# Optimization experiments

Measured on AMD Instinct MI355X. Metric: run time of the kernel, lower is better.

Reference implementation:

```python
import jax, jax.numpy as jnp
import numpy as np
import math

DIM = 768
NUM_HEADS = 16
PERHEAD = DIM // NUM_HEADS  # 48
B, T = 4, 2048


def setup_inputs() -> dict:
    key = jax.random.key(0)
    k_x, k_wi, k_bi, k_wo, k_bo = jax.random.split(key, 5)
    s_in = 1.0 / math.sqrt(DIM)
    return {
        "x": jax.random.normal(k_x, (B, T, DIM), dtype=jnp.float32),
        # linear_in: y = x @ w_in + b_in, w_in: (DIM, 3*DIM)
        "w_in": jax.random.uniform(k_wi, (DIM, 3 * DIM), jnp.float32, -s_in, s_in),
        "b_in": jax.random.uniform(k_bi, (3 * DIM,), jnp.float32, -s_in, s_in),
        "w_out": jax.random.uniform(k_wo, (DIM, DIM), jnp.float32, -s_in, s_in),
        "b_out": jax.random.uniform(k_bo, (DIM,), jnp.float32, -s_in, s_in),
    }


def reference(x, w_in, b_in, w_out, b_out):
    bs, tok, _ = x.shape
    qkv = x @ w_in + b_in                                   # (B, T, 3*DIM)
    # Faithful to torch: reshape to (B, T, H, 3*ph), move heads, chunk last dim.
    qkv = qkv.reshape(bs, tok, NUM_HEADS, 3 * PERHEAD)
    qkv = jnp.transpose(qkv, (0, 2, 1, 3))                  # (B, H, T, 3*ph)
    q, k, v = jnp.split(qkv, 3, axis=-1)                    # each (B, H, T, ph)
    scale = 1.0 / math.sqrt(PERHEAD)
    scores = jnp.einsum("bhqd,bhkd->bhqk", q, k) * scale    # (B, H, T, T)
    attn = jax.nn.softmax(scores, axis=-1)
    # dropout p=0.0 (eval) -> identity
    out = jnp.einsum("bhqk,bhkd->bhqd", attn, v)            # (B, H, T, ph)
    out = jnp.transpose(out, (0, 2, 1, 3)).reshape(bs, tok, DIM)
    return out @ w_out + b_out
```

## Files before the change

kernel.cpp:

```cpp
#include <hip/hip_runtime.h>
#include <hip/hip_bf16.h>
#include <math.h>

typedef __attribute__((ext_vector_type(8))) short short8;
typedef __attribute__((ext_vector_type(4))) float floatx4;
typedef __hip_bfloat16 bf16;

#define DIM 768
#define NHEADS 16
#define PH 48
#define VROWS 49
#define BATCH 4
#define SEQ 2048
#define MTOK (BATCH*SEQ)
#define NQKV (3*DIM)
#define NQK (2*DIM)
#define LOG2E 1.44269504088896f
#define CFAC (0.14433756729740643f * LOG2E)

#define NB_CAST   6144
#define NB_TWIN   1728
#define NB_TWOUT  576
#define NB_MISC   140

__device__ __forceinline__ void cp16(void* dst, const void* src) {
    *(float4*)dst = *(const float4*)src;
}
__device__ __forceinline__ unsigned short f2us(float v) {
    bf16 b = __float2bfloat16(v);
    return *(unsigned short*)&b;
}
__device__ __forceinline__ float us2f(unsigned short u) {
    bf16 b = *(bf16*)&u;
    return __bfloat162float(b);
}
__device__ __forceinline__ void gload_lds16(const bf16* g, bf16* l) {
    __builtin_amdgcn_global_load_lds(
        (const __attribute__((address_space(1))) unsigned int*)g,
        (__attribute__((address_space(3))) unsigned int*)l, 16, 0, 0);
}
__device__ __forceinline__ bool sniff_f32(const unsigned short* __restrict__ x) {
    float v = us2f(x[threadIdx.x & 63]);
    int bad = !(fabsf(v) < 64.0f);
    return __any(bad) != 0;
}

__global__ __launch_bounds__(256) void prep_all(
    const void* __restrict__ x, const void* __restrict__ w_in,
    const void* __restrict__ w_out, const void* __restrict__ bin,
    const void* __restrict__ bout,
    bf16* __restrict__ xb, bf16* __restrict__ winT, bf16* __restrict__ woutT,
    float* __restrict__ bi, float* __restrict__ bo, bf16* __restrict__ Vt)
{
    __shared__ bf16 tile[32][33];
    const int bid = blockIdx.x, tid = threadIdx.x;
    const bool f32 = sniff_f32((const unsigned short*)x);

    if (bid < NB_CAST) {
        int i = bid * 256 + tid;
        if (f32) {
            float4 v = ((const float4*)x)[i];
            ushort4 o;
            o.x = f2us(v.x); o.y = f2us(v.y); o.z = f2us(v.z); o.w = f2us(v.w);
            ((ushort4*)xb)[i] = o;
        } else {
            ((ushort4*)xb)[i] = ((const ushort4*)x)[i];
        }
    } else if (bid < NB_CAST + NB_TWIN + NB_TWOUT) {
        const void* in; bf16* out; int R, C, tt;
        if (bid < NB_CAST + NB_TWIN) {
            in = w_in; out = winT; R = DIM; C = NQKV; tt = bid - NB_CAST;
        } else {
            in = w_out; out = woutT; R = DIM; C = DIM; tt = bid - NB_CAST - NB_TWIN;
        }
        int ctiles = C / 32;
        int c0 = (tt % ctiles) * 32, r0 = (tt / ctiles) * 32;
        int tx = tid & 31, ty = tid >> 5;
#pragma unroll
        for (int j = 0; j < 4; j++) {
            size_t idx = (size_t)(r0 + ty + 8*j) * C + c0 + tx;
            float v = f32 ? ((const float*)in)[idx]
                          : us2f(((const unsigned short*)in)[idx]);
            tile[ty + 8*j][tx] = __float2bfloat16(v);
        }
        __syncthreads();
#pragma unroll
        for (int j = 0; j < 4; j++)
            out[(size_t)(c0 + ty + 8*j) * R + r0 + tx] = tile[tx][ty + 8*j];
    } else {
        int t = (bid - (NB_CAST + NB_TWIN + NB_TWOUT)) * 256 + tid;
        if (t < NQKV) {
            bi[t] = f32 ? ((const float*)bin)[t] : us2f(((const unsigned short*)bin)[t]);
        } else if (t < NQKV + DIM) {
            int j = t - NQKV;
            bo[j] = f32 ? ((const float*)bout)[j] : us2f(((const unsigned short*)bout)[j]);
        } else {
            int k = t - (NQKV + DIM);
            int bh = k >> 9, pos = (k & 511) * 4;
            bf16* dst = Vt + ((size_t)bh * VROWS + 48) * SEQ + pos;
            ushort4 ones;
            ones.x = ones.y = ones.z = ones.w = f2us(1.0f);
            *(ushort4*)dst = ones;
        }
    }
}

template<int N, int MODE>
__global__ __launch_bounds__(256) void gemm_bias(
    const bf16* __restrict__ A, const bf16* __restrict__ BT,
    const float* __restrict__ bias, void* __restrict__ C0, bf16* __restrict__ Vt,
    const unsigned short* __restrict__ xraw)
{
    constexpr int K = 768;
    __shared__ __align__(16) bf16 smem[2 * 128 * 32];
    bf16* As = smem;
    bf16* Bs = smem + 128 * 32;
    const bool out_f32 = (MODE == 2) && sniff_f32(xraw);
    const int tid = threadIdx.x;
    const int id = blockIdx.x;
    const int m0 = (id & 63) * 128, n0 = (id >> 6) * 128;
    const int w = tid >> 6, lane = tid & 63, lq = lane >> 4, ln = lane & 15;
    const int wr = w & 1, wc = w >> 1;

    const int rl0 = w * 32 + (lane >> 2);
    const int rl1 = rl0 + 16;
    const int ssw = ((lane >> 2) ^ (lane >> 4)) & 3;
    const int cm = (lane & 3) ^ ssw;
    const bf16* gA0 = A + (size_t)(m0 + rl0) * K + cm * 8;
    const bf16* gA1 = A + (size_t)(m0 + rl1) * K + cm * 8;
    const bf16* gB0 = BT + (size_t)(n0 + rl0) * K + cm * 8;
    const bf16* gB1 = BT + (size_t)(n0 + rl1) * K + cm * 8;
    bf16* lA0 = &As[(w * 32 + 0) * 32];
    bf16* lA1 = &As[(w * 32 + 16) * 32];
    bf16* lB0 = &Bs[(w * 32 + 0) * 32];
    bf16* lB1 = &Bs[(w * 32 + 16) * 32];

    const int rsw = (ln ^ (ln >> 2)) & 3;
    const int rchunk = (lq ^ rsw) * 8;

    floatx4 zero4 = {0.f, 0.f, 0.f, 0.f};
    floatx4 acc[4][4];
#pragma unroll
    for (int mi = 0; mi < 4; mi++)
#pragma unroll
        for (int nj = 0; nj < 4; nj++) acc[mi][nj] = zero4;

    for (int k0 = 0; k0 < K; k0 += 32) {
        gload_lds16(gA0, lA0);
        gload_lds16(gA1, lA1);
        gload_lds16(gB0, lB0);
        gload_lds16(gB1, lB1);
        gA0 += 32; gA1 += 32; gB0 += 32; gB1 += 32;
        __syncthreads();

        short8 a[4], b[4];
#pragma unroll
        for (int mi = 0; mi < 4; mi++)
            a[mi] = *(const short8*)&As[(wr * 64 + 16 * mi + ln) * 32 + rchunk];
#pragma unroll
        for (int nj = 0; nj < 4; nj++)
            b[nj] = *(const short8*)&Bs[(wc * 64 + 16 * nj + ln) * 32 + rchunk];
#pragma unroll
        for (int mi = 0; mi < 4; mi++)
#pragma unroll
            for (int nj = 0; nj < 4; nj++)
                acc[mi][nj] = __builtin_amdgcn_mfma_f32_16x16x32_bf16(
                    a[mi], b[nj], acc[mi][nj], 0, 0, 0);
        __syncthreads();
    }
    bf16 (*VLs)[136] = (bf16(*)[136])smem;

#pragma unroll
    for (int nj = 0; nj < 4; nj++) {
        int n = n0 + wc * 64 + 16 * nj + ln;
        float bv = bias[n];
        if (MODE == 2) {
#pragma unroll
            for (int mi = 0; mi < 4; mi++)
#pragma unroll
                for (int i = 0; i < 4; i++) {
                    size_t off = (size_t)(m0 + wr * 64 + 16 * mi + 4 * lq + i) * N + n;
                    float val = acc[mi][nj][i] + bv;
                    if (out_f32) ((float*)C0)[off] = val;
                    else         ((bf16*)C0)[off] = __float2bfloat16(val);
                }
        } else {
            int h = n / 144, r = n - 144 * h;
            if (r < 96) {
                float sc = (r < 48) ? CFAC : 1.0f;
#pragma unroll
                for (int mi = 0; mi < 4; mi++)
#pragma unroll
                    for (int i = 0; i < 4; i++) {
                        size_t off = (size_t)(m0 + wr * 64 + 16 * mi + 4 * lq + i) * NQK
                                     + h * 96 + r;
                        ((bf16*)C0)[off] = __float2bfloat16((acc[mi][nj][i] + bv) * sc);
                    }
            } else {
                int d = r - 96;
#pragma unroll
                for (int mi = 0; mi < 4; mi++)
#pragma unroll
                    for (int i = 0; i < 4; i++)
                        VLs[d][wr * 64 + 32 * (mi >> 1) + 8 * lq + 4 * (mi & 1) + i] =
                            __float2bfloat16(acc[mi][nj][i] + bv);
            }
        }
    }

    if (MODE == 1) {
        __syncthreads();
        const int bidx = m0 >> 11, tok0 = m0 & 2047;
#pragma unroll
        for (int s = 0; s < 3; s++) {
            int idx = tid + 256 * s;
            int d = idx >> 4, ch = idx & 15;
            int h = (n0 + 31 - d) / 144;
            int n = 144 * h + 96 + d;
            if (n >= n0 && n < n0 + 128) {
                bf16* dst = Vt + ((size_t)(bidx * NHEADS + h) * VROWS + d) * SEQ
                            + tok0 + ch * 8;
                *(float4*)dst = *(const float4*)&VLs[d][ch * 8];
            }
        }
    }
}

__global__ __launch_bounds__(256, 2) void attn_fused(
    const bf16* __restrict__ QK, const bf16* __restrict__ Vt, bf16* __restrict__ O)
{
    __shared__ bf16 Ks[2][64][72];
    __shared__ bf16 VsT[2][64][72];

    const int tid = threadIdx.x;
    const int id = blockIdx.x;
    const int g = id & 63, qt = id >> 6;
    const int h = g & 15, b = g >> 4;
    const int w = tid >> 6, lane = tid & 63, lq = lane >> 4, ln = lane & 15;
    const size_t rowbase = (size_t)b * SEQ;
    const int q0 = qt * 256;
    const int hoff = h * 96;
    const bf16* Vth = Vt + (size_t)(b * NHEADS + h) * VROWS * SEQ;

    const bf16 bzero = __float2bfloat16(0.f);
    for (int idx = tid; idx < 2048; idx += 256) {
        int bb = idx >> 10, r = (idx >> 4) & 63, c = idx & 15;
        Ks[bb][r][48 + c] = bzero;
    }

    short8 qa0[4], qa1[4];
    short8 zero8 = {0, 0, 0, 0, 0, 0, 0, 0};
#pragma unroll
    for (int f = 0; f < 4; f++) {
        const bf16* qrow = QK + (rowbase + q0 + 64*f + 16*w + ln) * NQK + hoff;
        qa0[f] = *(const short8*)(qrow + lq * 8);
        qa1[f] = (lq < 2) ? *(const short8*)(qrow + 32 + lq * 8) : zero8;
    }

    const int kr0a = tid / 6, kc0a = tid % 6;
    const int kr1a = (tid + 256) / 6, kc1a = (tid + 256) % 6;
    const char* kg0 = (const char*)(QK + (rowbase + kr0a) * NQK + hoff + 48) + kc0a * 16;
    const char* kg1 = (const char*)(QK + (rowbase + kr1a) * NQK + hoff + 48) + kc1a * 16;
    bf16* kd0 = &Ks[0][kr0a][kc0a * 8];
    bf16* kd1 = &Ks[0][kr1a & 63][kc1a * 8];
    const bool kact = (tid < 128);
    const int vr0 = tid >> 3, vc0 = tid & 7;
    const char* vg0 = (const char*)(Vth + (size_t)vr0 * SEQ) + vc0 * 16;
    const char* vg1 = (const char*)(Vth + (size_t)(32 + vr0) * SEQ) + vc0 * 16;
    bf16* vd0 = &VsT[0][vr0][vc0 * 8];
    bf16* vd1 = &VsT[0][32 + vr0][vc0 * 8];
    const bool vact = (tid < 136);
    const ptrdiff_t KADV = (ptrdiff_t)64 * NQK * 2;
    const ptrdiff_t VADV = 128;
    const int BOFF = 64 * 72;

    floatx4 zero4 = {0.f, 0.f, 0.f, 0.f};
    floatx4 o[4][4];
#pragma unroll
    for (int f = 0; f < 4; f++)
#pragma unroll
        for (int nt = 0; nt < 4; nt++) o[f][nt] = zero4;

    float4 rk0, rk1, rv0, rv1;
    rk0 = *(const float4*)kg0;
    if (kact) rk1 = *(const float4*)kg1;
    rv0 = *(const float4*)vg0;
    if (vact) rv1 = *(const float4*)vg1;
    kg0 += KADV; kg1 += KADV; vg0 += VADV; vg1 += VADV;
    *(float4*)kd0 = rk0;
    if (kact) *(float4*)kd1 = rk1;
    *(float4*)vd0 = rv0;
    if (vact) *(float4*)vd1 = rv1;
    rk0 = *(const float4*)kg0;
    if (kact) rk1 = *(const float4*)kg1;
    rv0 = *(const float4*)vg0;
    if (vact) rv1 = *(const float4*)vg1;
    kg0 += KADV; kg1 += KADV; vg0 += VADV; vg1 += VADV;
    __syncthreads();

    for (int kt = 0; kt < 32; kt++) {
        const int cur = kt & 1;
        if (kt < 31) {
            const int nb = (cur ^ 1) * BOFF;
            *(float4*)(kd0 + nb) = rk0;
            if (kact) *(float4*)(kd1 + nb) = rk1;
            *(float4*)(vd0 + nb) = rv0;
            if (vact) *(float4*)(vd1 + nb) = rv1;
            if (kt < 30) {
                rk0 = *(const float4*)kg0;
                if (kact) rk1 = *(const float4*)kg1;
                rv0 = *(const float4*)vg0;
                if (vact) rv1 = *(const float4*)vg1;
                kg0 += KADV; kg1 += KADV; vg0 += VADV; vg1 += VADV;
            }
        }

        const bf16 (*Kc)[72] = Ks[cur];
        const bf16 (*Vc)[72] = VsT[cur];

        __builtin_amdgcn_s_setprio(1);
        short8 kb0[4], kb1[4];
#pragma unroll
        for (int t = 0; t < 4; t++) {
            kb0[t] = *(const short8*)&Kc[16*t + ln][lq * 8];
            kb1[t] = *(const short8*)&Kc[16*t + ln][lq * 8 + 32];
        }

        short8 pa[4][2];
#pragma unroll
        for (int f = 0; f < 4; f++) {
            floatx4 s[4];
#pragma unroll
            for (int t = 0; t < 4; t++) s[t] = zero4;
#pragma unroll
            for (int t = 0; t < 4; t++) {
                s[t] = __builtin_amdgcn_mfma_f32_16x16x32_bf16(kb0[t], qa0[f], s[t], 0, 0, 0);
                s[t] = __builtin_amdgcn_mfma_f32_16x16x32_bf16(kb1[t], qa1[f], s[t], 0, 0, 0);
            }
#pragma unroll
            for (int ks = 0; ks < 2; ks++) {
                union { short8 v; __hip_bfloat162 h2[4]; } u;
                float2 p;
                p.x = __builtin_amdgcn_exp2f(s[2*ks][0]);
                p.y = __builtin_amdgcn_exp2f(s[2*ks][1]);
                u.h2[0] = __float22bfloat162_rn(p);
                p.x = __builtin_amdgcn_exp2f(s[2*ks][2]);
                p.y = __builtin_amdgcn_exp2f(s[2*ks][3]);
                u.h2[1] = __float22bfloat162_rn(p);
                p.x = __builtin_amdgcn_exp2f(s[2*ks+1][0]);
                p.y = __builtin_amdgcn_exp2f(s[2*ks+1][1]);
                u.h2[2] = __float22bfloat162_rn(p);
                p.x = __builtin_amdgcn_exp2f(s[2*ks+1][2]);
                p.y = __builtin_amdgcn_exp2f(s[2*ks+1][3]);
                u.h2[3] = __float22bfloat162_rn(p);
                pa[f][ks] = u.v;
            }
        }

#pragma unroll
        for (int nt = 0; nt < 4; nt++) {
            short8 vb0 = *(const short8*)&Vc[16*nt + ln][lq * 8];
            short8 vb1 = *(const short8*)&Vc[16*nt + ln][lq * 8 + 32];
#pragma unroll
            for (int f = 0; f < 4; f++) {
                o[f][nt] = __builtin_amdgcn_mfma_f32_16x16x32_bf16(pa[f][0], vb0, o[f][nt], 0, 0, 0);
                o[f][nt] = __builtin_amdgcn_mfma_f32_16x16x32_bf16(pa[f][1], vb1, o[f][nt], 0, 0, 0);
            }
        }
        __builtin_amdgcn_s_setprio(0);
        __syncthreads();
    }

#pragma unroll
    for (int f = 0; f < 4; f++)
#pragma unroll
        for (int i = 0; i < 4; i++) {
            float l = __shfl(o[f][3][i], (lane >> 4) << 4);
            float inv = 1.0f / l;
            int row = q0 + 64*f + 16*w + 4*lq + i;
#pragma unroll
            for (int nt = 0; nt < 3; nt++)
                O[(rowbase + row) * DIM + h * PH + 16*nt + ln] =
                    __float2bfloat16(o[f][nt][i] * inv);
        }
}

extern "C" void kernel_launch(void* const* d_in, const int* in_sizes, int n_in,
                              void* d_out, int out_size, void* d_ws, size_t ws_size,
                              hipStream_t stream) {
    const void* x     = d_in[0];
    const void* w_in  = d_in[1];
    const void* b_in  = d_in[2];
    const void* w_out = d_in[3];
    const void* b_out = d_in[4];

    bf16* qk    = (bf16*)d_ws;
    bf16* Vt    = qk    + (size_t)MTOK * NQK;
    bf16* xb    = Vt    + (size_t)BATCH * NHEADS * VROWS * SEQ;
    bf16* attn  = xb;
    bf16* winT  = xb    + (size_t)MTOK * DIM;
    bf16* woutT = winT  + (size_t)NQKV * DIM;
    float* bi   = (float*)(woutT + (size_t)DIM * DIM);
    float* bo   = bi + NQKV;

    prep_all<<<NB_CAST + NB_TWIN + NB_TWOUT + NB_MISC, 256, 0, stream>>>(
        x, w_in, w_out, b_in, b_out, xb, winT, woutT, bi, bo, Vt);

    gemm_bias<NQKV, 1><<<64 * (NQKV/128), 256, 0, stream>>>(
        xb, winT, bi, qk, Vt, (const unsigned short*)x);
    attn_fused<<<64 * (SEQ/256), 256, 0, stream>>>(qk, Vt, attn);
    gemm_bias<DIM, 2><<<64 * (DIM/128), 256, 0, stream>>>(
        attn, woutT, bo, d_out, nullptr, (const unsigned short*)x);
}
```

Measured before the change: 212.4 us.

## Use BK=64 GEMM tiles, smaller M-tile for out-proj, explicit softmax row sums

The GEMM main loop now loads two 32-wide K slices per barrier pair, which halves the number of syncs, and the tile height is a template parameter. The output projection uses 64-row tiles so it launches twice as many blocks. In attention, the ones-row trick that computed softmax denominators through an extra MFMA column tile is replaced by accumulating the exp values in registers and reducing them with shuffles. This drops a quarter of the PV MFMAs and the matching V loads, at the cost of extra VALU adds and more LDS per GEMM block.

```diff
diff --git a/kernel.cpp b/kernel.cpp
--- a/kernel.cpp
+++ b/kernel.cpp
@@ -105,67 +105,84 @@
     }
 }
 
-template<int N, int MODE>
+template<int N, int MODE, int TM>
 __global__ __launch_bounds__(256) void gemm_bias(
     const bf16* __restrict__ A, const bf16* __restrict__ BT,
     const float* __restrict__ bias, void* __restrict__ C0, bf16* __restrict__ Vt,
     const unsigned short* __restrict__ xraw)
 {
     constexpr int K = 768;
-    __shared__ __align__(16) bf16 smem[2 * 128 * 32];
-    bf16* As = smem;
-    bf16* Bs = smem + 128 * 32;
+    constexpr int MI = TM / 32;
+    constexpr int TS = TM * 32;
+    constexpr int BS = 128 * 32;
+    __shared__ __align__(16) bf16 smem[2 * TS + 2 * BS];
+    bf16* As0 = smem;
+    bf16* As1 = smem + TS;
+    bf16* Bs0 = smem + 2 * TS;
+    bf16* Bs1 = smem + 2 * TS + BS;
     const bool out_f32 = (MODE == 2) && sniff_f32(xraw);
     const int tid = threadIdx.x;
     const int id = blockIdx.x;
-    const int m0 = (id & 63) * 128, n0 = (id >> 6) * 128;
+    constexpr int NMB = MTOK / TM;
+    const int m0 = (id % NMB) * TM, n0 = (id / NMB) * 128;
     const int w = tid >> 6, lane = tid & 63, lq = lane >> 4, ln = lane & 15;
     const int wr = w & 1, wc = w >> 1;
 
-    const int rl0 = w * 32 + (lane >> 2);
-    const int rl1 = rl0 + 16;
     const int ssw = ((lane >> 2) ^ (lane >> 4)) & 3;
     const int cm = (lane & 3) ^ ssw;
-    const bf16* gA0 = A + (size_t)(m0 + rl0) * K + cm * 8;
-    const bf16* gA1 = A + (size_t)(m0 + rl1) * K + cm * 8;
-    const bf16* gB0 = BT + (size_t)(n0 + rl0) * K + cm * 8;
-    const bf16* gB1 = BT + (size_t)(n0 + rl1) * K + cm * 8;
-    bf16* lA0 = &As[(w * 32 + 0) * 32];
-    bf16* lA1 = &As[(w * 32 + 16) * 32];
-    bf16* lB0 = &Bs[(w * 32 + 0) * 32];
-    bf16* lB1 = &Bs[(w * 32 + 16) * 32];
+    const int rlB0 = w * 32 + (lane >> 2), rlB1 = rlB0 + 16;
+    const int rlA  = (TM == 128) ? rlB0 : (w * 16 + (lane >> 2));
+    const bf16* gA0 = A + (size_t)(m0 + rlA) * K + cm * 8;
+    const bf16* gA1 = A + (size_t)(m0 + rlA + ((TM == 128) ? 16 : 0)) * K + cm * 8;
+    const bf16* gB0 = BT + (size_t)(n0 + rlB0) * K + cm * 8;
+    const bf16* gB1 = BT + (size_t)(n0 + rlB1) * K + cm * 8;
+    bf16* lA0 = As0 + ((TM == 128) ? (w * 32) * 32 : (w * 16) * 32);
+    bf16* lA1 = As0 + (w * 32 + 16) * 32;
+    bf16* lB0 = Bs0 + (w * 32) * 32;
+    bf16* lB1 = Bs0 + (w * 32 + 16) * 32;
 
     const int rsw = (ln ^ (ln >> 2)) & 3;
     const int rchunk = (lq ^ rsw) * 8;
 
     floatx4 zero4 = {0.f, 0.f, 0.f, 0.f};
-    floatx4 acc[4][4];
-#pragma unroll
-    for (int mi = 0; mi < 4; mi++)
+    floatx4 acc[MI][4];
+#pragma unroll
+    for (int mi = 0; mi < MI; mi++)
 #pragma unroll
         for (int nj = 0; nj < 4; nj++) acc[mi][nj] = zero4;
 
-    for (int k0 = 0; k0 < K; k0 += 32) {
-        gload_lds16(gA0, lA0);
-        gload_lds16(gA1, lA1);
-        gload_lds16(gB0, lB0);
-        gload_lds16(gB1, lB1);
-        gA0 += 32; gA1 += 32; gB0 += 32; gB1 += 32;
+    for (int k0 = 0; k0 < K; k0 += 64) {
+        gload_lds16(gA0,      lA0);
+        gload_lds16(gA0 + 32, lA0 + TS);
+        if constexpr (TM == 128) {
+            gload_lds16(gA1,      lA1);
+            gload_lds16(gA1 + 32, lA1 + TS);
+        }
+        gload_lds16(gB0,      lB0);
+        gload_lds16(gB0 + 32, lB0 + BS);
+        gload_lds16(gB1,      lB1);
+        gload_lds16(gB1 + 32, lB1 + BS);
+        gA0 += 64; gA1 += 64; gB0 += 64; gB1 += 64;
         __syncthreads();
 
-        short8 a[4], b[4];
-#pragma unroll
-        for (int mi = 0; mi < 4; mi++)
-            a[mi] = *(const short8*)&As[(wr * 64 + 16 * mi + ln) * 32 + rchunk];
-#pragma unroll
-        for (int nj = 0; nj < 4; nj++)
-            b[nj] = *(const short8*)&Bs[(wc * 64 + 16 * nj + ln) * 32 + rchunk];
-#pragma unroll
-        for (int mi = 0; mi < 4; mi++)
+#pragma unroll
+        for (int kk = 0; kk < 2; kk++) {
+            const bf16* Asub = kk ? As1 : As0;
+            const bf16* Bsub = kk ? Bs1 : Bs0;
+            short8 a[MI], b[4];
+#pragma unroll
+            for (int mi = 0; mi < MI; mi++)
+                a[mi] = *(const short8*)&Asub[(wr * (TM/2) + 16 * mi + ln) * 32 + rchunk];
 #pragma unroll
             for (int nj = 0; nj < 4; nj++)
-                acc[mi][nj] = __builtin_amdgcn_mfma_f32_16x16x32_bf16(
-                    a[mi], b[nj], acc[mi][nj], 0, 0, 0);
+                b[nj] = *(const short8*)&Bsub[(wc * 64 + 16 * nj + ln) * 32 + rchunk];
+#pragma unroll
+            for (int mi = 0; mi < MI; mi++)
+#pragma unroll
+                for (int nj = 0; nj < 4; nj++)
+                    acc[mi][nj] = __builtin_amdgcn_mfma_f32_16x16x32_bf16(
+                        a[mi], b[nj], acc[mi][nj], 0, 0, 0);
+        }
         __syncthreads();
     }
     bf16 (*VLs)[136] = (bf16(*)[136])smem;
@@ -176,10 +193,10 @@
         float bv = bias[n];
         if (MODE == 2) {
 #pragma unroll
-            for (int mi = 0; mi < 4; mi++)
+            for (int mi = 0; mi < MI; mi++)
 #pragma unroll
                 for (int i = 0; i < 4; i++) {
-                    size_t off = (size_t)(m0 + wr * 64 + 16 * mi + 4 * lq + i) * N + n;
+                    size_t off = (size_t)(m0 + wr * (TM/2) + 16 * mi + 4 * lq + i) * N + n;
                     float val = acc[mi][nj][i] + bv;
                     if (out_f32) ((float*)C0)[off] = val;
                     else         ((bf16*)C0)[off] = __float2bfloat16(val);
@@ -189,17 +206,17 @@
             if (r < 96) {
                 float sc = (r < 48) ? CFAC : 1.0f;
 #pragma unroll
-                for (int mi = 0; mi < 4; mi++)
+                for (int mi = 0; mi < MI; mi++)
 #pragma unroll
                     for (int i = 0; i < 4; i++) {
-                        size_t off = (size_t)(m0 + wr * 64 + 16 * mi + 4 * lq + i) * NQK
+                        size_t off = (size_t)(m0 + wr * (TM/2) + 16 * mi + 4 * lq + i) * NQK
                                      + h * 96 + r;
                         ((bf16*)C0)[off] = __float2bfloat16((acc[mi][nj][i] + bv) * sc);
                     }
             } else {
                 int d = r - 96;
 #pragma unroll
-                for (int mi = 0; mi < 4; mi++)
+                for (int mi = 0; mi < MI; mi++)
 #pragma unroll
                     for (int i = 0; i < 4; i++)
                         VLs[d][wr * 64 + 32 * (mi >> 1) + 8 * lq + 4 * (mi & 1) + i] =
@@ -269,17 +286,18 @@
     const char* vg1 = (const char*)(Vth + (size_t)(32 + vr0) * SEQ) + vc0 * 16;
     bf16* vd0 = &VsT[0][vr0][vc0 * 8];
     bf16* vd1 = &VsT[0][32 + vr0][vc0 * 8];
-    const bool vact = (tid < 136);
+    const bool vact = (tid < 128);
     const ptrdiff_t KADV = (ptrdiff_t)64 * NQK * 2;
     const ptrdiff_t VADV = 128;
     const int BOFF = 64 * 72;
 
     floatx4 zero4 = {0.f, 0.f, 0.f, 0.f};
-    floatx4 o[4][4];
+    floatx4 o[4][3];
+    float dsum[4] = {0.f, 0.f, 0.f, 0.f};
 #pragma unroll
     for (int f = 0; f < 4; f++)
 #pragma unroll
-        for (int nt = 0; nt < 4; nt++) o[f][nt] = zero4;
+        for (int nt = 0; nt < 3; nt++) o[f][nt] = zero4;
 
     float4 rk0, rk1, rv0, rv1;
     rk0 = *(const float4*)kg0;
@@ -339,26 +357,27 @@
             }
 #pragma unroll
             for (int ks = 0; ks < 2; ks++) {
+                float e0 = __builtin_amdgcn_exp2f(s[2*ks][0]);
+                float e1 = __builtin_amdgcn_exp2f(s[2*ks][1]);
+                float e2 = __builtin_amdgcn_exp2f(s[2*ks][2]);
+                float e3 = __builtin_amdgcn_exp2f(s[2*ks][3]);
+                float e4 = __builtin_amdgcn_exp2f(s[2*ks+1][0]);
+                float e5 = __builtin_amdgcn_exp2f(s[2*ks+1][1]);
+                float e6 = __builtin_amdgcn_exp2f(s[2*ks+1][2]);
+                float e7 = __builtin_amdgcn_exp2f(s[2*ks+1][3]);
+                dsum[f] += ((e0 + e1) + (e2 + e3)) + ((e4 + e5) + (e6 + e7));
                 union { short8 v; __hip_bfloat162 h2[4]; } u;
                 float2 p;
-                p.x = __builtin_amdgcn_exp2f(s[2*ks][0]);
-                p.y = __builtin_amdgcn_exp2f(s[2*ks][1]);
-                u.h2[0] = __float22bfloat162_rn(p);
-                p.x = __builtin_amdgcn_exp2f(s[2*ks][2]);
-                p.y = __builtin_amdgcn_exp2f(s[2*ks][3]);
-                u.h2[1] = __float22bfloat162_rn(p);
-                p.x = __builtin_amdgcn_exp2f(s[2*ks+1][0]);
-                p.y = __builtin_amdgcn_exp2f(s[2*ks+1][1]);
-                u.h2[2] = __float22bfloat162_rn(p);
-                p.x = __builtin_amdgcn_exp2f(s[2*ks+1][2]);
-                p.y = __builtin_amdgcn_exp2f(s[2*ks+1][3]);
-                u.h2[3] = __float22bfloat162_rn(p);
+                p.x = e0; p.y = e1; u.h2[0] = __float22bfloat162_rn(p);
+                p.x = e2; p.y = e3; u.h2[1] = __float22bfloat162_rn(p);
+                p.x = e4; p.y = e5; u.h2[2] = __float22bfloat162_rn(p);
+                p.x = e6; p.y = e7; u.h2[3] = __float22bfloat162_rn(p);
                 pa[f][ks] = u.v;
             }
         }
 
 #pragma unroll
-        for (int nt = 0; nt < 4; nt++) {
+        for (int nt = 0; nt < 3; nt++) {
             short8 vb0 = *(const short8*)&Vc[16*nt + ln][lq * 8];
             short8 vb1 = *(const short8*)&Vc[16*nt + ln][lq * 8 + 32];
 #pragma unroll
@@ -372,10 +391,13 @@
     }
 
 #pragma unroll
-    for (int f = 0; f < 4; f++)
+    for (int f = 0; f < 4; f++) {
+        float dtot = dsum[f];
+        dtot += __shfl_xor(dtot, 16);
+        dtot += __shfl_xor(dtot, 32);
 #pragma unroll
         for (int i = 0; i < 4; i++) {
-            float l = __shfl(o[f][3][i], (lane >> 4) << 4);
+            float l = __shfl(dtot, 4*lq + i);
             float inv = 1.0f / l;
             int row = q0 + 64*f + 16*w + 4*lq + i;
 #pragma unroll
@@ -383,6 +405,7 @@
                 O[(rowbase + row) * DIM + h * PH + 16*nt + ln] =
                     __float2bfloat16(o[f][nt][i] * inv);
         }
+    }
 }
 
 extern "C" void kernel_launch(void* const* d_in, const int* in_sizes, int n_in,
@@ -406,9 +429,9 @@
     prep_all<<<NB_CAST + NB_TWIN + NB_TWOUT + NB_MISC, 256, 0, stream>>>(
         x, w_in, w_out, b_in, b_out, xb, winT, woutT, bi, bo, Vt);
 
-    gemm_bias<NQKV, 1><<<64 * (NQKV/128), 256, 0, stream>>>(
+    gemm_bias<NQKV, 1, 128><<<64 * (NQKV/128), 256, 0, stream>>>(
         xb, winT, bi, qk, Vt, (const unsigned short*)x);
     attn_fused<<<64 * (SEQ/256), 256, 0, stream>>>(qk, Vt, attn);
-    gemm_bias<DIM, 2><<<64 * (DIM/128), 256, 0, stream>>>(
+    gemm_bias<DIM, 2, 64><<<128 * (DIM/128), 256, 0, stream>>>(
         attn, woutT, bo, d_out, nullptr, (const unsigned short*)x);
 }
```

Result: no change. 215.6 us (+1.5%).
